# Kernel tuning notes

Hardware: AMD Instinct MI355X
Metric: run time of the kernel (lower is better)

Reference implementation:

```python
import jax, jax.numpy as jnp
import numpy as np

N = 50000       # nodes
E = 800000      # edges (avg degree 16)
F_IN = 128      # num_node_features
H = 128         # hidden_dim
C = 16          # num_classes
G = 512         # graphs in batch


def setup_inputs() -> dict:
    key = jax.random.key(0)
    ks = jax.random.split(key, 12)
    x = jax.random.normal(ks[0], (N, F_IN), dtype=jnp.float32)
    edge_index = jax.random.randint(ks[1], (2, E), 0, N, dtype=jnp.int32)
    batch = jnp.sort(jax.random.randint(ks[2], (N,), 0, G, dtype=jnp.int32))
    def lin(k, fan_in, shape):
        bound = 1.0 / np.sqrt(fan_in)
        return jax.random.uniform(k, shape, jnp.float32, -bound, bound)
    # SAGEConv1: lin_l (aggr, with bias), lin_r (root, no bias)
    w1l = lin(ks[3], F_IN, (F_IN, H)); b1 = lin(ks[4], F_IN, (H,))
    w1r = lin(ks[5], F_IN, (F_IN, H))
    # SAGEConv2
    w2l = lin(ks[6], H, (H, H)); b2 = lin(ks[7], H, (H,))
    w2r = lin(ks[8], H, (H, H))
    # final fc
    wf = lin(ks[9], H, (H, C)); bf = lin(ks[10], H, (C,))
    return {"x": x, "edge_index": edge_index, "batch": batch,
            "w1l": w1l, "b1": b1, "w1r": w1r,
            "w2l": w2l, "b2": b2, "w2r": w2r,
            "wf": wf, "bf": bf}


def _sage_conv(x, src, dst, wl, bl, wr):
    # mean-aggregate source-node features at destination nodes
    msg_sum = jax.ops.segment_sum(x[src], dst, num_segments=N)      # [N, d]
    cnt = jax.ops.segment_sum(jnp.ones((src.shape[0], 1), x.dtype), dst,
                              num_segments=N)                        # [N, 1]
    aggr = msg_sum / jnp.maximum(cnt, 1.0)
    return aggr @ wl + bl + x @ wr


def reference(x, edge_index, batch, w1l, b1, w1r, w2l, b2, w2r, wf, bf):
    src, dst = edge_index[0], edge_index[1]
    h = jax.nn.relu(_sage_conv(x, src, dst, w1l, b1, w1r))
    # dropout(p=0.5) is identity at inference
    h = jax.nn.relu(_sage_conv(h, src, dst, w2l, b2, w2r))
    # global_mean_pool over graph ids
    gsum = jax.ops.segment_sum(h, batch, num_segments=G)             # [G, H]
    gcnt = jax.ops.segment_sum(jnp.ones((N, 1), h.dtype), batch,
                               num_segments=G)                        # [G, 1]
    g = gsum / jnp.maximum(gcnt, 1.0)
    logits = g @ wf + bf
    return jax.nn.log_softmax(logits, axis=1)
```

## Files before the change

kernel.cpp:

```cpp
#include <hip/hip_runtime.h>
#include <hip/hip_bf16.h>
#include <math.h>


#define FDIM 128

typedef __attribute__((ext_vector_type(8))) short bf16x8;
typedef __attribute__((ext_vector_type(4))) float f32x4;

__device__ inline unsigned short f2bf(float f) {
    union { float f; unsigned u; } v; v.f = f;
    unsigned r = v.u + 0x7fff + ((v.u >> 16) & 1);
    return (unsigned short)(r >> 16);
}
__device__ inline float bf2f(unsigned short b) {
    union { unsigned u; float f; } v; v.u = ((unsigned)b) << 16;
    return v.f;
}

__global__ __launch_bounds__(256) void prep_k(
        const int* __restrict__ dst, int* __restrict__ deg, int* __restrict__ rank, int nE,
        const float* __restrict__ x, unsigned short* __restrict__ xb, int n4,
        const float* __restrict__ w1l, const float* __restrict__ w1r,
        unsigned short* __restrict__ wp1,
        const float* __restrict__ w2l, const float* __restrict__ w2r,
        unsigned short* __restrict__ wp2,
        int nbE, int nbC) {
    int bid = blockIdx.x, tid = threadIdx.x;
    if (bid < nbE) {
        int e = bid * 256 + tid;
        if (e < nE) rank[e] = atomicAdd(&deg[dst[e]], 1);
    } else if (bid < nbE + nbC) {
        int i = (bid - nbE) * 256 + tid;
        if (i < n4) {
            float4 v = ((const float4*)x)[i];
            ushort4 o;
            o.x = f2bf(v.x); o.y = f2bf(v.y); o.z = f2bf(v.z); o.w = f2bf(v.w);
            ((ushort4*)xb)[i] = o;
        }
    } else {
        int pb = bid - nbE - nbC;
        const float* wl = (pb < 16) ? w1l : w2l;
        const float* wr = (pb < 16) ? w1r : w2r;
        unsigned short* wp = (pb < 16) ? wp1 : wp2;
        int t = (pb & 15) * 256 + tid;
        int lane = t & 63, s = (t >> 6) & 7, nt = t >> 9;
        int kbase = s * 32 + ((lane >> 4) * 8);
        int c = nt * 16 + (lane & 15);
        unsigned short tmp[8];
        #pragma unroll
        for (int j = 0; j < 8; ++j) {
            int k = kbase + j;
            float w = (k < 128) ? wl[k * 128 + c] : wr[(k - 128) * 128 + c];
            tmp[j] = f2bf(w);
        }
        ushort4 lo, hi;
        lo.x = tmp[0]; lo.y = tmp[1]; lo.z = tmp[2]; lo.w = tmp[3];
        hi.x = tmp[4]; hi.y = tmp[5]; hi.z = tmp[6]; hi.w = tmp[7];
        ((ushort4*)wp)[t * 2 + 0] = lo;
        ((ushort4*)wp)[t * 2 + 1] = hi;
    }
}

__global__ __launch_bounds__(256) void scan1_k(const int* __restrict__ deg,
                                               int* __restrict__ rowstart,
                                               int* __restrict__ bsum, int n) {
    __shared__ int s[256];
    int tid = threadIdx.x;
    int i = blockIdx.x * 256 + tid;
    int v = (i < n) ? deg[i] : 0;
    s[tid] = v;
    __syncthreads();
    for (int off = 1; off < 256; off <<= 1) {
        int t = (tid >= off) ? s[tid - off] : 0;
        __syncthreads();
        s[tid] += t;
        __syncthreads();
    }
    if (i < n) rowstart[i] = s[tid] - v;
    if (tid == 255) bsum[blockIdx.x] = s[255];
}

__global__ __launch_bounds__(256) void scan2_k(int* __restrict__ bsum, int nb) {
    __shared__ int s[256];
    int tid = threadIdx.x;
    int v = (tid < nb) ? bsum[tid] : 0;
    s[tid] = v;
    __syncthreads();
    for (int off = 1; off < 256; off <<= 1) {
        int t = (tid >= off) ? s[tid - off] : 0;
        __syncthreads();
        s[tid] += t;
        __syncthreads();
    }
    if (tid < nb) bsum[tid] = s[tid] - v;
}

__global__ void addoff_k(int* __restrict__ rowstart, const int* __restrict__ bsum, int n) {
    int i = blockIdx.x * blockDim.x + threadIdx.x;
    if (i < n) rowstart[i] += bsum[blockIdx.x];
}

__global__ __launch_bounds__(256) void fill_swz_k(
        const int* __restrict__ src, const int* __restrict__ dst,
        const int* __restrict__ rowstart, const int* __restrict__ rank,
        int* __restrict__ csr, int nE, int rngSize) {
    int cls = blockIdx.x & 7;
    int lo = cls * rngSize, hi = lo + rngSize;
    int nb = gridDim.x >> 3;
    int bi = blockIdx.x >> 3;
    for (int e = bi * 256 + threadIdx.x; e < nE; e += nb * 256) {
        int d = dst[e];
        if (d >= lo && d < hi)
            csr[rowstart[d] + rank[e]] = src[e];
    }
}

__global__ __launch_bounds__(256) void gather_cls_k(
        const uint2* __restrict__ feat,
        const int* __restrict__ csr, const int* __restrict__ rowstart,
        const int* __restrict__ deg, uint2* __restrict__ outr,
        int n, int perHalf) {
    int b = blockIdx.x;
    int xcd = b & 7;
    int cls = xcd & 3;
    int grp = (b >> 3) + ((xcd >> 2) ? perHalf : 0);
    int wave = threadIdx.x >> 6, lane = threadIdx.x & 63;
    int es = lane >> 3, cs = lane & 7;
    int colOff = cls * 8 + cs;

    int nodeA = grp * 8 + wave * 2;
    int nodeB = nodeA + 1;
    int sA = 0, dA = 0, sB = 0, dB = 0;
    if (nodeA < n) { sA = rowstart[nodeA]; dA = deg[nodeA]; }
    if (nodeB < n) { sB = rowstart[nodeB]; dB = deg[nodeB]; }

    float a0 = 0.f, a1 = 0.f, a2 = 0.f, a3 = 0.f;
    float b0 = 0.f, b1 = 0.f, b2 = 0.f, b3 = 0.f;
    int dmax = max(dA, dB);
    for (int base = 0; base < dmax; base += 16) {
        int e0 = base + es, e1 = base + 8 + es;
        int iA0 = (e0 < dA) ? csr[sA + e0] : -1;
        int iA1 = (e1 < dA) ? csr[sA + e1] : -1;
        int iB0 = (e0 < dB) ? csr[sB + e0] : -1;
        int iB1 = (e1 < dB) ? csr[sB + e1] : -1;
        uint2 wA0 = feat[(size_t)max(iA0, 0) * 32 + colOff];
        uint2 wA1 = feat[(size_t)max(iA1, 0) * 32 + colOff];
        uint2 wB0 = feat[(size_t)max(iB0, 0) * 32 + colOff];
        uint2 wB1 = feat[(size_t)max(iB1, 0) * 32 + colOff];
        if (iA0 < 0) { wA0.x = 0; wA0.y = 0; }
        if (iA1 < 0) { wA1.x = 0; wA1.y = 0; }
        if (iB0 < 0) { wB0.x = 0; wB0.y = 0; }
        if (iB1 < 0) { wB1.x = 0; wB1.y = 0; }
        a0 += bf2f((unsigned short)(wA0.x & 0xffff)) + bf2f((unsigned short)(wA1.x & 0xffff));
        a1 += bf2f((unsigned short)(wA0.x >> 16))    + bf2f((unsigned short)(wA1.x >> 16));
        a2 += bf2f((unsigned short)(wA0.y & 0xffff)) + bf2f((unsigned short)(wA1.y & 0xffff));
        a3 += bf2f((unsigned short)(wA0.y >> 16))    + bf2f((unsigned short)(wA1.y >> 16));
        b0 += bf2f((unsigned short)(wB0.x & 0xffff)) + bf2f((unsigned short)(wB1.x & 0xffff));
        b1 += bf2f((unsigned short)(wB0.x >> 16))    + bf2f((unsigned short)(wB1.x >> 16));
        b2 += bf2f((unsigned short)(wB0.y & 0xffff)) + bf2f((unsigned short)(wB1.y & 0xffff));
        b3 += bf2f((unsigned short)(wB0.y >> 16))    + bf2f((unsigned short)(wB1.y >> 16));
    }
    #pragma unroll
    for (int m = 8; m <= 32; m <<= 1) {
        a0 += __shfl_xor(a0, m, 64); a1 += __shfl_xor(a1, m, 64);
        a2 += __shfl_xor(a2, m, 64); a3 += __shfl_xor(a3, m, 64);
        b0 += __shfl_xor(b0, m, 64); b1 += __shfl_xor(b1, m, 64);
        b2 += __shfl_xor(b2, m, 64); b3 += __shfl_xor(b3, m, 64);
    }

    if (es == 0) {
        if (nodeA < n) {
            float inv = (dA > 0) ? 1.0f / (float)dA : 0.0f;
            uint2 o;
            o.x = ((unsigned)f2bf(a1 * inv) << 16) | (unsigned)f2bf(a0 * inv);
            o.y = ((unsigned)f2bf(a3 * inv) << 16) | (unsigned)f2bf(a2 * inv);
            outr[(size_t)nodeA * 32 + colOff] = o;
        }
        if (nodeB < n) {
            float inv = (dB > 0) ? 1.0f / (float)dB : 0.0f;
            uint2 o;
            o.x = ((unsigned)f2bf(b1 * inv) << 16) | (unsigned)f2bf(b0 * inv);
            o.y = ((unsigned)f2bf(b3 * inv) << 16) | (unsigned)f2bf(b2 * inv);
            outr[(size_t)nodeB * 32 + colOff] = o;
        }
    }
}

__global__ __launch_bounds__(256) void gemm_mfma_k(
        const unsigned short* __restrict__ A,
        const unsigned short* __restrict__ R,
        const unsigned short* __restrict__ wp,
        const float* __restrict__ bias,
        unsigned short* __restrict__ outp,
        int n) {
    int tid = threadIdx.x;
    int wave = tid >> 6, lane = tid & 63;
    int rowTile = blockIdx.x * 64 + wave * 16;
    int lrow = lane & 15, lk = lane >> 4;

    int arow = rowTile + lrow;
    if (arow >= n) arow = n - 1;

    bf16x8 a[8];
    const unsigned short* abase = A + (size_t)arow * FDIM + lk * 8;
    const unsigned short* rbase = R + (size_t)arow * FDIM + lk * 8;
    #pragma unroll
    for (int s = 0; s < 4; ++s) a[s] = *(const bf16x8*)(abase + s * 32);
    #pragma unroll
    for (int s = 0; s < 4; ++s) a[4 + s] = *(const bf16x8*)(rbase + s * 32);

    const bf16x8* bp = (const bf16x8*)wp;
    int ocol = lane & 15;
    int orow0 = rowTile + (lane >> 4) * 4;

    #pragma unroll
    for (int nt = 0; nt < 8; ++nt) {
        float bv = bias[nt * 16 + ocol];
        f32x4 acc = {bv, bv, bv, bv};
        #pragma unroll
        for (int s = 0; s < 8; ++s) {
            bf16x8 b = bp[(nt * 8 + s) * 64 + lane];
            acc = __builtin_amdgcn_mfma_f32_16x16x32_bf16(a[s], b, acc, 0, 0, 0);
        }
        #pragma unroll
        for (int r = 0; r < 4; ++r) {
            int orow = orow0 + r;
            if (orow < n) {
                float v = fmaxf(acc[r], 0.0f);
                outp[(size_t)orow * FDIM + nt * 16 + ocol] = f2bf(v);
            }
        }
    }
}

__global__ __launch_bounds__(256) void pool_seg_k(
        const unsigned short* __restrict__ h,
        const int* __restrict__ batch,
        float* __restrict__ gsum, int* __restrict__ gcnt, int nN) {
    __shared__ int bw[64];
    __shared__ float red[8][32][4];
    int base = blockIdx.x * 64;
    if (base >= nN) return;
    int tid = threadIdx.x;
    int rg = tid >> 5, cs = tid & 31;
    int cnt = min(64, nN - base);
    if (tid < 64) bw[tid] = batch[min(base + tid, nN - 1)];
    __syncthreads();
    int g0 = bw[0], g1 = bw[cnt - 1];

    for (int g = g0; g <= g1; ++g) {
        int s = 0;
        while (s < cnt && bw[s] < g) ++s;
        int e = s;
        while (e < cnt && bw[e] == g) ++e;

        float a0 = 0.f, a1 = 0.f, a2 = 0.f, a3 = 0.f;
        for (int i = s + rg; i < e; i += 8) {
            uint2 v = ((const uint2*)(h + (size_t)(base + i) * FDIM))[cs];
            a0 += bf2f((unsigned short)(v.x & 0xffff));
            a1 += bf2f((unsigned short)(v.x >> 16));
            a2 += bf2f((unsigned short)(v.y & 0xffff));
            a3 += bf2f((unsigned short)(v.y >> 16));
        }
        red[rg][cs][0] = a0; red[rg][cs][1] = a1;
        red[rg][cs][2] = a2; red[rg][cs][3] = a3;
        __syncthreads();
        if (rg == 0 && e > s) {
            #pragma unroll
            for (int r = 1; r < 8; ++r) {
                a0 += red[r][cs][0]; a1 += red[r][cs][1];
                a2 += red[r][cs][2]; a3 += red[r][cs][3];
            }
            float* go = gsum + (size_t)g * FDIM + cs * 4;
            atomicAdd(go + 0, a0);
            atomicAdd(go + 1, a1);
            atomicAdd(go + 2, a2);
            atomicAdd(go + 3, a3);
            if (cs == 0) atomicAdd(&gcnt[g], e - s);
        }
        __syncthreads();
    }
}

__global__ __launch_bounds__(128) void head_k(const float* __restrict__ gsum,
                                              const int* __restrict__ gcnt,
                                              const float* __restrict__ wf,
                                              const float* __restrict__ bf,
                                              float* __restrict__ out, int nG) {
    int g = blockIdx.x;
    if (g >= nG) return;
    __shared__ float row[FDIM];
    int tid = threadIdx.x;
    float inv = 1.0f / fmaxf((float)gcnt[g], 1.0f);
    row[tid] = gsum[(size_t)g * FDIM + tid] * inv;
    __syncthreads();

    float logit = -1e30f;
    if (tid < 16) {
        logit = bf[tid];
        for (int k = 0; k < FDIM; ++k) logit += row[k] * wf[k * 16 + tid];
    }
    float m = logit;
    for (int off = 8; off >= 1; off >>= 1) m = fmaxf(m, __shfl_xor(m, off, 64));
    float ev = (tid < 16) ? expf(logit - m) : 0.0f;
    float sum = ev;
    for (int off = 8; off >= 1; off >>= 1) sum += __shfl_xor(sum, off, 64);
    if (tid < 16) out[(size_t)g * 16 + tid] = logit - m - logf(sum);
}

extern "C" void kernel_launch(void* const* d_in, const int* in_sizes, int n_in,
                              void* d_out, int out_size, void* d_ws, size_t ws_size,
                              hipStream_t stream) {
    const float* x    = (const float*)d_in[0];
    const int*   ei   = (const int*)d_in[1];
    const int*   batch= (const int*)d_in[2];
    const float* w1l  = (const float*)d_in[3];
    const float* b1   = (const float*)d_in[4];
    const float* w1r  = (const float*)d_in[5];
    const float* w2l  = (const float*)d_in[6];
    const float* b2   = (const float*)d_in[7];
    const float* w2r  = (const float*)d_in[8];
    const float* wf   = (const float*)d_in[9];
    const float* bf   = (const float*)d_in[10];
    float* out = (float*)d_out;

    const int N = in_sizes[0] / FDIM;
    const int E = in_sizes[1] / 2;
    const int G = out_size / 16;
    const int* src = ei;
    const int* dst = ei + E;
    const int NB = (N + 255) / 256;

    char* ws = (char*)d_ws;
    size_t off = 0;
    auto alloc = [&](size_t bytes) { void* p = ws + off; off = (off + bytes + 255) & ~(size_t)255; return p; };
    unsigned short* xb   = (unsigned short*)alloc((size_t)N * FDIM * 2);
    unsigned short* aggr = (unsigned short*)alloc((size_t)N * FDIM * 2);
    unsigned short* h1   = (unsigned short*)alloc((size_t)N * FDIM * 2);
    unsigned short* wp1  = (unsigned short*)alloc(8 * 8 * 64 * 8 * 2);
    unsigned short* wp2  = (unsigned short*)alloc(8 * 8 * 64 * 8 * 2);
    int* deg      = (int*)alloc((size_t)N * sizeof(int));
    int* rowstart = (int*)alloc((size_t)N * sizeof(int));
    int* bsum     = (int*)alloc(256 * sizeof(int));
    int* csr      = (int*)alloc((size_t)E * sizeof(int));
    int* rank     = (int*)alloc((size_t)E * sizeof(int));
    float* gsum   = (float*)alloc((size_t)G * FDIM * sizeof(float));
    int*   gcnt   = (int*)alloc((size_t)G * sizeof(int));
    unsigned short* h2 = xb;

    hipMemsetAsync(deg, 0, (size_t)N * sizeof(int), stream);
    hipMemsetAsync(gsum, 0, (size_t)G * FDIM * sizeof(float), stream);
    hipMemsetAsync(gcnt, 0, (size_t)G * sizeof(int), stream);

    const int nbE = (E + 255) / 256;
    const int nbC = (N * FDIM / 4 + 255) / 256;
    prep_k<<<nbE + nbC + 32, 256, 0, stream>>>(dst, deg, rank, E,
                                               x, xb, N * FDIM / 4,
                                               w1l, w1r, wp1, w2l, w2r, wp2,
                                               nbE, nbC);

    scan1_k<<<NB, 256, 0, stream>>>(deg, rowstart, bsum, N);
    scan2_k<<<1, 256, 0, stream>>>(bsum, NB);
    addoff_k<<<NB, 256, 0, stream>>>(rowstart, bsum, N);
    {
        int rngSize = (N + 7) / 8;
        fill_swz_k<<<2048, 256, 0, stream>>>(src, dst, rowstart, rank, csr, E, rngSize);
    }

    const int nGrpTot = (N + 7) / 8;
    const int perHalf = (nGrpTot + 1) / 2;
    const int gatherGrid = 8 * perHalf;

    gather_cls_k<<<gatherGrid, 256, 0, stream>>>((const uint2*)xb, csr, rowstart, deg,
                                                 (uint2*)aggr, N, perHalf);
    gemm_mfma_k<<<(N + 63) / 64, 256, 0, stream>>>(aggr, xb, wp1, b1, h1, N);

    gather_cls_k<<<gatherGrid, 256, 0, stream>>>((const uint2*)h1, csr, rowstart, deg,
                                                 (uint2*)aggr, N, perHalf);
    gemm_mfma_k<<<(N + 63) / 64, 256, 0, stream>>>(aggr, h1, wp2, b2, h2, N);

    pool_seg_k<<<(N + 63) / 64, 256, 0, stream>>>(h2, batch, gsum, gcnt, N);
    head_k<<<G, 128, 0, stream>>>(gsum, gcnt, wf, bf, out, G);
}
```

Measured before the change: 218.9 us.

## Rewrite neighbor gather as one-wave-per-node with 16-byte loads and index prefetch

Replaces the XCD-class-split gather, where each wave handled two nodes and a quarter of the columns with 8-byte loads, with a kernel in which each wave handles one node across all 128 columns using 16-byte uint4 loads. The CSR indices for the next 16 edges are prefetched while the current feature loads are in flight, and the tail is handled with clamped indices and a zero multiplier instead of branches. The aim is fewer, wider memory transactions and more loads in flight per wave. It gives up the per-XCD column partitioning that may have improved L2 locality, and a node with a short tail still issues full-width padded loads.

```diff
diff --git a/kernel.cpp b/kernel.cpp
--- a/kernel.cpp
+++ b/kernel.cpp
@@ -16,6 +16,29 @@
 __device__ inline float bf2f(unsigned short b) {
     union { unsigned u; float f; } v; v.u = ((unsigned)b) << 16;
     return v.f;
+}
+
+__device__ inline void acc8(float* a, uint4 w) {
+    union { unsigned u; float f; } t;
+    t.u = w.x << 16;          a[0] += t.f;
+    t.u = w.x & 0xffff0000u;  a[1] += t.f;
+    t.u = w.y << 16;          a[2] += t.f;
+    t.u = w.y & 0xffff0000u;  a[3] += t.f;
+    t.u = w.z << 16;          a[4] += t.f;
+    t.u = w.z & 0xffff0000u;  a[5] += t.f;
+    t.u = w.w << 16;          a[6] += t.f;
+    t.u = w.w & 0xffff0000u;  a[7] += t.f;
+}
+__device__ inline void acc8m(float* a, uint4 w, float m) {
+    union { unsigned u; float f; } t;
+    t.u = w.x << 16;          a[0] = fmaf(m, t.f, a[0]);
+    t.u = w.x & 0xffff0000u;  a[1] = fmaf(m, t.f, a[1]);
+    t.u = w.y << 16;          a[2] = fmaf(m, t.f, a[2]);
+    t.u = w.y & 0xffff0000u;  a[3] = fmaf(m, t.f, a[3]);
+    t.u = w.z << 16;          a[4] = fmaf(m, t.f, a[4]);
+    t.u = w.z & 0xffff0000u;  a[5] = fmaf(m, t.f, a[5]);
+    t.u = w.w << 16;          a[6] = fmaf(m, t.f, a[6]);
+    t.u = w.w & 0xffff0000u;  a[7] = fmaf(m, t.f, a[7]);
 }
 
 __global__ __launch_bounds__(256) void prep_k(
@@ -116,74 +139,74 @@
     }
 }
 
-__global__ __launch_bounds__(256) void gather_cls_k(
-        const uint2* __restrict__ feat,
+__global__ __launch_bounds__(256) void gather_v4_k(
+        const uint4* __restrict__ feat,
         const int* __restrict__ csr, const int* __restrict__ rowstart,
-        const int* __restrict__ deg, uint2* __restrict__ outr,
-        int n, int perHalf) {
-    int b = blockIdx.x;
-    int xcd = b & 7;
-    int cls = xcd & 3;
-    int grp = (b >> 3) + ((xcd >> 2) ? perHalf : 0);
-    int wave = threadIdx.x >> 6, lane = threadIdx.x & 63;
-    int es = lane >> 3, cs = lane & 7;
-    int colOff = cls * 8 + cs;
-
-    int nodeA = grp * 8 + wave * 2;
-    int nodeB = nodeA + 1;
-    int sA = 0, dA = 0, sB = 0, dB = 0;
-    if (nodeA < n) { sA = rowstart[nodeA]; dA = deg[nodeA]; }
-    if (nodeB < n) { sB = rowstart[nodeB]; dB = deg[nodeB]; }
-
-    float a0 = 0.f, a1 = 0.f, a2 = 0.f, a3 = 0.f;
-    float b0 = 0.f, b1 = 0.f, b2 = 0.f, b3 = 0.f;
-    int dmax = max(dA, dB);
-    for (int base = 0; base < dmax; base += 16) {
-        int e0 = base + es, e1 = base + 8 + es;
-        int iA0 = (e0 < dA) ? csr[sA + e0] : -1;
-        int iA1 = (e1 < dA) ? csr[sA + e1] : -1;
-        int iB0 = (e0 < dB) ? csr[sB + e0] : -1;
-        int iB1 = (e1 < dB) ? csr[sB + e1] : -1;
-        uint2 wA0 = feat[(size_t)max(iA0, 0) * 32 + colOff];
-        uint2 wA1 = feat[(size_t)max(iA1, 0) * 32 + colOff];
-        uint2 wB0 = feat[(size_t)max(iB0, 0) * 32 + colOff];
-        uint2 wB1 = feat[(size_t)max(iB1, 0) * 32 + colOff];
-        if (iA0 < 0) { wA0.x = 0; wA0.y = 0; }
-        if (iA1 < 0) { wA1.x = 0; wA1.y = 0; }
-        if (iB0 < 0) { wB0.x = 0; wB0.y = 0; }
-        if (iB1 < 0) { wB1.x = 0; wB1.y = 0; }
-        a0 += bf2f((unsigned short)(wA0.x & 0xffff)) + bf2f((unsigned short)(wA1.x & 0xffff));
-        a1 += bf2f((unsigned short)(wA0.x >> 16))    + bf2f((unsigned short)(wA1.x >> 16));
-        a2 += bf2f((unsigned short)(wA0.y & 0xffff)) + bf2f((unsigned short)(wA1.y & 0xffff));
-        a3 += bf2f((unsigned short)(wA0.y >> 16))    + bf2f((unsigned short)(wA1.y >> 16));
-        b0 += bf2f((unsigned short)(wB0.x & 0xffff)) + bf2f((unsigned short)(wB1.x & 0xffff));
-        b1 += bf2f((unsigned short)(wB0.x >> 16))    + bf2f((unsigned short)(wB1.x >> 16));
-        b2 += bf2f((unsigned short)(wB0.y & 0xffff)) + bf2f((unsigned short)(wB1.y & 0xffff));
-        b3 += bf2f((unsigned short)(wB0.y >> 16))    + bf2f((unsigned short)(wB1.y >> 16));
-    }
+        const int* __restrict__ deg, uint4* __restrict__ outr, int n) {
+    int node = blockIdx.x * 4 + (threadIdx.x >> 6);
+    if (node >= n) return;
+    int lane = threadIdx.x & 63;
+    int es = lane >> 4;
+    int cs = lane & 15;
+    int s0 = rowstart[node], dc = deg[node];
+
+    float acc[8] = {0.f, 0.f, 0.f, 0.f, 0.f, 0.f, 0.f, 0.f};
+    int base = 0;
+    int i0 = 0, i1 = 0, i2 = 0, i3 = 0;
+    if (base + 16 <= dc) {
+        i0 = csr[s0 + es];
+        i1 = csr[s0 + 4 + es];
+        i2 = csr[s0 + 8 + es];
+        i3 = csr[s0 + 12 + es];
+    }
+    while (base + 16 <= dc) {
+        uint4 w0 = feat[(size_t)i0 * 16 + cs];
+        uint4 w1 = feat[(size_t)i1 * 16 + cs];
+        uint4 w2 = feat[(size_t)i2 * 16 + cs];
+        uint4 w3 = feat[(size_t)i3 * 16 + cs];
+        base += 16;
+        if (base + 16 <= dc) {
+            i0 = csr[s0 + base + es];
+            i1 = csr[s0 + base + 4 + es];
+            i2 = csr[s0 + base + 8 + es];
+            i3 = csr[s0 + base + 12 + es];
+        }
+        acc8(acc, w0);
+        acc8(acc, w1);
+        acc8(acc, w2);
+        acc8(acc, w3);
+    }
+    if (base < dc) {
+        int c = dc - 1;
+        int e0 = base + es, e1 = base + 4 + es, e2 = base + 8 + es, e3 = base + 12 + es;
+        int t0 = csr[s0 + min(e0, c)];
+        int t1 = csr[s0 + min(e1, c)];
+        int t2 = csr[s0 + min(e2, c)];
+        int t3 = csr[s0 + min(e3, c)];
+        uint4 w0 = feat[(size_t)t0 * 16 + cs];
+        uint4 w1 = feat[(size_t)t1 * 16 + cs];
+        uint4 w2 = feat[(size_t)t2 * 16 + cs];
+        uint4 w3 = feat[(size_t)t3 * 16 + cs];
+        acc8m(acc, w0, (e0 < dc) ? 1.0f : 0.0f);
+        acc8m(acc, w1, (e1 < dc) ? 1.0f : 0.0f);
+        acc8m(acc, w2, (e2 < dc) ? 1.0f : 0.0f);
+        acc8m(acc, w3, (e3 < dc) ? 1.0f : 0.0f);
+    }
+
     #pragma unroll
-    for (int m = 8; m <= 32; m <<= 1) {
-        a0 += __shfl_xor(a0, m, 64); a1 += __shfl_xor(a1, m, 64);
-        a2 += __shfl_xor(a2, m, 64); a3 += __shfl_xor(a3, m, 64);
-        b0 += __shfl_xor(b0, m, 64); b1 += __shfl_xor(b1, m, 64);
-        b2 += __shfl_xor(b2, m, 64); b3 += __shfl_xor(b3, m, 64);
+    for (int k = 0; k < 8; ++k) {
+        acc[k] += __shfl_xor(acc[k], 16, 64);
+        acc[k] += __shfl_xor(acc[k], 32, 64);
     }
 
     if (es == 0) {
-        if (nodeA < n) {
-            float inv = (dA > 0) ? 1.0f / (float)dA : 0.0f;
-            uint2 o;
-            o.x = ((unsigned)f2bf(a1 * inv) << 16) | (unsigned)f2bf(a0 * inv);
-            o.y = ((unsigned)f2bf(a3 * inv) << 16) | (unsigned)f2bf(a2 * inv);
-            outr[(size_t)nodeA * 32 + colOff] = o;
-        }
-        if (nodeB < n) {
-            float inv = (dB > 0) ? 1.0f / (float)dB : 0.0f;
-            uint2 o;
-            o.x = ((unsigned)f2bf(b1 * inv) << 16) | (unsigned)f2bf(b0 * inv);
-            o.y = ((unsigned)f2bf(b3 * inv) << 16) | (unsigned)f2bf(b2 * inv);
-            outr[(size_t)nodeB * 32 + colOff] = o;
-        }
+        float inv = (dc > 0) ? 1.0f / (float)dc : 0.0f;
+        uint4 o;
+        o.x = ((unsigned)f2bf(acc[1] * inv) << 16) | (unsigned)f2bf(acc[0] * inv);
+        o.y = ((unsigned)f2bf(acc[3] * inv) << 16) | (unsigned)f2bf(acc[2] * inv);
+        o.z = ((unsigned)f2bf(acc[5] * inv) << 16) | (unsigned)f2bf(acc[4] * inv);
+        o.w = ((unsigned)f2bf(acc[7] * inv) << 16) | (unsigned)f2bf(acc[6] * inv);
+        outr[(size_t)node * 16 + cs] = o;
     }
 }
 
@@ -368,16 +391,12 @@
         fill_swz_k<<<2048, 256, 0, stream>>>(src, dst, rowstart, rank, csr, E, rngSize);
     }
 
-    const int nGrpTot = (N + 7) / 8;
-    const int perHalf = (nGrpTot + 1) / 2;
-    const int gatherGrid = 8 * perHalf;
-
-    gather_cls_k<<<gatherGrid, 256, 0, stream>>>((const uint2*)xb, csr, rowstart, deg,
-                                                 (uint2*)aggr, N, perHalf);
+    gather_v4_k<<<(N + 3) / 4, 256, 0, stream>>>((const uint4*)xb, csr, rowstart, deg,
+                                                 (uint4*)aggr, N);
     gemm_mfma_k<<<(N + 63) / 64, 256, 0, stream>>>(aggr, xb, wp1, b1, h1, N);
 
-    gather_cls_k<<<gatherGrid, 256, 0, stream>>>((const uint2*)h1, csr, rowstart, deg,
-                                                 (uint2*)aggr, N, perHalf);
+    gather_v4_k<<<(N + 3) / 4, 256, 0, stream>>>((const uint4*)h1, csr, rowstart, deg,
+                                                 (uint4*)aggr, N);
     gemm_mfma_k<<<(N + 63) / 64, 256, 0, stream>>>(aggr, h1, wp2, b2, h2, N);
 
     pool_seg_k<<<(N + 63) / 64, 256, 0, stream>>>(h2, batch, gsum, gcnt, N);
```

Result: faster. 177.1 us (-19.1%).
